# Optimization experiments

Measured on AMD Instinct MI355X. Metric: run time of the kernel, lower is better.

The kernel has to match this reference:

```python
import jax, jax.numpy as jnp
import numpy as np

NFEAT, NHID, NCLASS = 256, 128, 40
N_NODES, N_EDGES = 50000, 800000
BN_EPS = 1e-5


def setup_inputs() -> dict:
    key = jax.random.key(0)
    ks = jax.random.split(key, 8)
    x = jax.random.normal(ks[0], (N_NODES, NFEAT), dtype=jnp.float32)
    edge_index = jax.random.randint(ks[1], (2, N_EDGES), 0, N_NODES, dtype=jnp.int64)
    # GCNConv layer 0: nfeat -> nhid (Glorot-ish scale)
    W0 = jax.random.normal(ks[2], (NFEAT, NHID), dtype=jnp.float32) / np.sqrt(NFEAT)
    b0 = jnp.zeros((NHID,), dtype=jnp.float32)
    # BatchNorm1d(nhid)
    gamma0 = jnp.ones((NHID,), dtype=jnp.float32)
    beta0 = jnp.zeros((NHID,), dtype=jnp.float32)
    # GCNConv last: nhid -> nclass
    W1 = jax.random.normal(ks[3], (NHID, NCLASS), dtype=jnp.float32) / np.sqrt(NHID)
    b1 = jnp.zeros((NCLASS,), dtype=jnp.float32)
    return {"x": x, "edge_index": edge_index, "W0": W0, "b0": b0,
            "gamma0": gamma0, "beta0": beta0, "W1": W1, "b1": b1}


def _gcn_conv(x, src, dst, W, b, num_nodes):
    # normalize=False GCNConv: linear transform then raw sum aggregation src->dst
    h = x @ W                                   # [N, out]
    out = jax.ops.segment_sum(h[src], dst, num_segments=num_nodes)
    return out + b


def reference(x, edge_index, W0, b0, gamma0, beta0, W1, b1):
    N = x.shape[0]
    src, dst = edge_index[0], edge_index[1]
    # layer 0 conv
    h = _gcn_conv(x, src, dst, W0, b0, N)       # [N, nhid]
    # BatchNorm1d (training-mode batch stats, biased variance)
    mu = h.mean(axis=0)
    var = jnp.mean((h - mu) ** 2, axis=0)
    h = gamma0 * (h - mu) * jax.lax.rsqrt(var + BN_EPS) + beta0
    h = jax.nn.relu(h)
    # (dropout skipped: deterministic eval baseline)
    # last conv (early-return path in original forward)
    out = _gcn_conv(h, src, dst, W1, b1, N)     # [N, nclass]
    return out
```

## Files before the change

kernel.cpp:

```cpp
#include <hip/hip_runtime.h>
#include <hip/hip_fp8.h>

#define NFEAT 256
#define NHID 128
#define NCLASS 40
#define NNODES 50000
#define NEDGES 800000
#define BN_EPS 1e-5f
#define NBK 196
#define NBLK 100
#define EPB 8000
#define BKCAP 6144
#define NW1 6250
#define GEMM1_BLOCKS 1563

typedef __attribute__((ext_vector_type(4))) float f32x4;
typedef __attribute__((ext_vector_type(8))) short bf16x8;

__device__ inline ushort f2bf(float f) {
    uint u = __float_as_uint(f);
    u += 0x7FFF + ((u >> 16) & 1);
    return (ushort)(u >> 16);
}
__device__ inline float bflo(uint v) { return __uint_as_float(v << 16); }
__device__ inline float bfhi(uint v) { return __uint_as_float(v & 0xFFFF0000u); }

__device__ inline uint pk_fp8x4(float a0, float a1, float a2, float a3) {
#if __has_builtin(__builtin_amdgcn_cvt_pk_fp8_f32)
    int u = 0;
    u = __builtin_amdgcn_cvt_pk_fp8_f32(a0, a1, u, false);
    u = __builtin_amdgcn_cvt_pk_fp8_f32(a2, a3, u, true);
    return (uint)u;
#else
    __hip_fp8_e4m3 q0(a0), q1(a1), q2(a2), q3(a3);
    return (uint)q0.__x | ((uint)q1.__x << 8) | ((uint)q2.__x << 16) | ((uint)q3.__x << 24);
#endif
}
__device__ inline float fp8lo(uint v) {
#if __has_builtin(__builtin_amdgcn_cvt_f32_fp8)
    return __builtin_amdgcn_cvt_f32_fp8((int)v, 0);
#else
    __hip_fp8_e4m3 q; q.__x = (__hip_fp8_storage_t)(v & 0xFF); return (float)q;
#endif
}
__device__ inline float fp8hi(uint v) {
#if __has_builtin(__builtin_amdgcn_cvt_f32_fp8)
    return __builtin_amdgcn_cvt_f32_fp8((int)v, 1);
#else
    __hip_fp8_e4m3 q; q.__x = (__hip_fp8_storage_t)((v >> 8) & 0xFF); return (float)q;
#endif
}

__global__ void k_prep(const float* __restrict__ W0, ushort* __restrict__ W0F,
                       const int* __restrict__ ei, int* __restrict__ bcnt) {
    __shared__ int cnt[NBK];
    if (blockIdx.x < 16) {
        const int t = blockIdx.x * 256 + threadIdx.x;
        const int lane = t & 63;
        const int grp = t >> 6;
        const int kc = grp & 7, fi = grp >> 3;
        const int n = fi * 16 + (lane & 15);
        const int k0 = kc * 32 + (lane >> 4) * 8;
        ushort v[8];
        #pragma unroll
        for (int j = 0; j < 8; ++j) v[j] = f2bf(W0[(k0 + j) * NHID + n]);
        uint4 u;
        u.x = (uint)v[0] | ((uint)v[1] << 16);
        u.y = (uint)v[2] | ((uint)v[3] << 16);
        u.z = (uint)v[4] | ((uint)v[5] << 16);
        u.w = (uint)v[6] | ((uint)v[7] << 16);
        *(uint4*)&W0F[(grp * 64 + lane) * 8] = u;
    } else {
        const int blk = blockIdx.x - 16;
        const int t = threadIdx.x;
        if (t < NBK) cnt[t] = 0;
        __syncthreads();
        const int base = blk * EPB;
        for (int i = t; i < EPB; i += 256)
            atomicAdd(&cnt[ei[NEDGES + base + i] >> 8], 1);
        __syncthreads();
        if (t < NBK) bcnt[blk * NBK + t] = cnt[t];
    }
}

__global__ void k_bkscan(const int* __restrict__ bcnt, int* __restrict__ off,
                         int* __restrict__ bstart, int* __restrict__ rowptr,
                         float* __restrict__ stats) {
    __shared__ int sc[256];
    const int t = threadIdx.x;
    stats[t] = 0.f;
    int tot = 0;
    if (t < NBK)
        for (int b = 0; b < NBLK; ++b) tot += bcnt[b * NBK + t];
    sc[t] = tot;
    __syncthreads();
    for (int o = 1; o < 256; o <<= 1) {
        const int v = (t >= o) ? sc[t - o] : 0;
        __syncthreads();
        sc[t] += v;
        __syncthreads();
    }
    const int excl = sc[t] - tot;
    if (t < NBK) bstart[t] = excl;
    else if (t == NBK) bstart[NBK] = sc[NBK - 1];
    if (t == 0) rowptr[NNODES] = NEDGES;
    if (t < NBK) {
        int run = excl;
        for (int b = 0; b < NBLK; ++b) { off[b * NBK + t] = run; run += bcnt[b * NBK + t]; }
    }
}

__launch_bounds__(256)
__global__ void k_scatter_gemm1(const int* __restrict__ ei, const int* __restrict__ off,
                                uint* __restrict__ packed,
                                const float* __restrict__ x, const ushort* __restrict__ W0F,
                                uchar* __restrict__ h1) {
    __shared__ int cur[NBK];
    if (blockIdx.x < NBLK) {
        const int t = threadIdx.x, blk = blockIdx.x;
        if (t < NBK) cur[t] = off[blk * NBK + t];
        __syncthreads();
        const int base = blk * EPB;
        for (int i = t; i < EPB; i += 256) {
            const int src = ei[base + i];
            const int dst = ei[NEDGES + base + i];
            const int pos = atomicAdd(&cur[dst >> 8], 1);
            packed[pos] = (uint)src | ((uint)(dst & 255) << 16);
        }
    } else {
        const int gt = (blockIdx.x - NBLK) * 256 + threadIdx.x;
        const int w = gt >> 6;
        if (w >= NW1) return;
        const int lane = gt & 63;
        const int half = w & 1;
        const int node = (w >> 1) * 16 + (lane & 15);
        const int nclamp = node < NNODES ? node : NNODES - 1;
        const float* xg = &x[(long)nclamp * NFEAT + (lane >> 4) * 8];

        float4 xa[8], xb[8];
        #pragma unroll
        for (int kc = 0; kc < 8; ++kc) {
            xa[kc] = *(const float4*)(xg + kc * 32);
            xb[kc] = *(const float4*)(xg + kc * 32 + 4);
        }
        __builtin_amdgcn_sched_barrier(0);
        bf16x8 xf[8];
        #pragma unroll
        for (int kc = 0; kc < 8; ++kc) {
            xf[kc][0]=(short)f2bf(xa[kc].x); xf[kc][1]=(short)f2bf(xa[kc].y);
            xf[kc][2]=(short)f2bf(xa[kc].z); xf[kc][3]=(short)f2bf(xa[kc].w);
            xf[kc][4]=(short)f2bf(xb[kc].x); xf[kc][5]=(short)f2bf(xb[kc].y);
            xf[kc][6]=(short)f2bf(xb[kc].z); xf[kc][7]=(short)f2bf(xb[kc].w);
        }
        __builtin_amdgcn_sched_barrier(0);
        f32x4 acc[4];
        #pragma unroll
        for (int f = 0; f < 4; ++f) acc[f] = (f32x4){0.f, 0.f, 0.f, 0.f};
        const ushort* wbase = &W0F[(size_t)lane * 8];
        #pragma unroll
        for (int kc = 0; kc < 8; ++kc) {
            #pragma unroll
            for (int f = 0; f < 4; ++f) {
                const int grp = (half * 4 + f) * 8 + kc;
                const bf16x8 wf = *(const bf16x8*)&wbase[(size_t)grp * 64 * 8];
                acc[f] = __builtin_amdgcn_mfma_f32_16x16x32_bf16(wf, xf[kc], acc[f], 0, 0, 0);
            }
        }
        if (node < NNODES) {
            const int nq = (lane >> 4) * 4;
            uchar* hp = &h1[(long)node * NHID + half * 64 + nq];
            #pragma unroll
            for (int f = 0; f < 4; ++f)
                *(uint*)&hp[f * 16] = pk_fp8x4(acc[f][0], acc[f][1], acc[f][2], acc[f][3]);
        }
    }
}

__launch_bounds__(256)
__global__ void k_bksort(const uint* __restrict__ packed, const int* __restrict__ bstart,
                         int* __restrict__ esrc, int* __restrict__ rowptr) {
    __shared__ uint pr[BKCAP];
    __shared__ int cnt[256], sc[256], cur[256];
    const int t = threadIdx.x, b = blockIdx.x;
    const int nb = bstart[b], ne = bstart[b + 1];
    const int n = ne - nb;
    cnt[t] = 0;
    __syncthreads();
    for (int i = t; i < n; i += 256) {
        const uint p = packed[nb + i];
        pr[i] = p;
        atomicAdd(&cnt[p >> 16], 1);
    }
    __syncthreads();
    const int v = cnt[t];
    sc[t] = v;
    __syncthreads();
    for (int o = 1; o < 256; o <<= 1) {
        const int tmp = (t >= o) ? sc[t - o] : 0;
        __syncthreads();
        sc[t] += tmp;
        __syncthreads();
    }
    const int excl = sc[t] - v;
    cur[t] = excl;
    const int node = (b << 8) + t;
    if (node < NNODES) rowptr[node] = nb + excl;
    __syncthreads();
    for (int i = t; i < n; i += 256) {
        const uint p = pr[i];
        const int pos = atomicAdd(&cur[p >> 16], 1);
        esrc[nb + pos] = (int)(p & 0xFFFFu);
    }
}

__launch_bounds__(256)
__global__ void k_gather1(const int* __restrict__ rowptr, const int* __restrict__ esrc,
                          const uchar* __restrict__ h1, const float* __restrict__ b0,
                          float* __restrict__ agg1) {
    const int w = (blockIdx.x * blockDim.x + threadIdx.x) >> 6;
    const int lane = threadIdx.x & 63;
    if (w >= NNODES) return;
    const int beg = rowptr[w], end = rowptr[w + 1];
    const int f = lane * 2;
    float2 acc = *(const float2*)&b0[f];
    int i = beg;
    for (; i + 7 < end; i += 8) {
        uint v[8];
        #pragma unroll
        for (int j = 0; j < 8; ++j)
            v[j] = (uint)*(const ushort*)&h1[(long)esrc[i + j] * NHID + f];
        #pragma unroll
        for (int j = 0; j < 8; ++j) { acc.x += fp8lo(v[j]); acc.y += fp8hi(v[j]); }
    }
    for (; i < end; ++i) {
        const uint v = (uint)*(const ushort*)&h1[(long)esrc[i] * NHID + f];
        acc.x += fp8lo(v); acc.y += fp8hi(v);
    }
    *(float2*)&agg1[(long)w * NHID + f] = acc;
}

__global__ void k_bnstats(const float* __restrict__ agg1,
                          float* __restrict__ sums, float* __restrict__ sumsq) {
    __shared__ float sd[256 * 4], sd2[256 * 4];
    const int t = threadIdx.x;
    const int c4 = (t & 31) * 4;
    const int rr = t >> 5;
    float4 s = make_float4(0.f,0.f,0.f,0.f), s2 = s;
    for (int r = blockIdx.x * 8 + rr; r < NNODES; r += gridDim.x * 8) {
        const float4 v = *(const float4*)&agg1[(long)r * NHID + c4];
        s.x += v.x; s.y += v.y; s.z += v.z; s.w += v.w;
        s2.x += v.x*v.x; s2.y += v.y*v.y; s2.z += v.z*v.z; s2.w += v.w*v.w;
    }
    *(float4*)&sd[t * 4] = s; *(float4*)&sd2[t * 4] = s2;
    __syncthreads();
    if (t < 32) {
        #pragma unroll
        for (int j = 1; j < 8; ++j) {
            const float4 a = *(const float4*)&sd[(j * 32 + t) * 4];
            const float4 a2 = *(const float4*)&sd2[(j * 32 + t) * 4];
            s = *(float4*)&sd[t * 4];
            s2 = *(float4*)&sd2[t * 4];
            s.x += a.x; s.y += a.y; s.z += a.z; s.w += a.w;
            s2.x += a2.x; s2.y += a2.y; s2.z += a2.z; s2.w += a2.w;
            *(float4*)&sd[t * 4] = s; *(float4*)&sd2[t * 4] = s2;
        }
        atomicAdd(&sums[c4 + 0], s.x);  atomicAdd(&sums[c4 + 1], s.y);
        atomicAdd(&sums[c4 + 2], s.z);  atomicAdd(&sums[c4 + 3], s.w);
        atomicAdd(&sumsq[c4 + 0], s2.x); atomicAdd(&sumsq[c4 + 1], s2.y);
        atomicAdd(&sumsq[c4 + 2], s2.z); atomicAdd(&sumsq[c4 + 3], s2.w);
    }
}

__launch_bounds__(256)
__global__ void k_gemm2(const float* __restrict__ agg1, const float* __restrict__ W1,
                        const float* __restrict__ sums, const float* __restrict__ sumsq,
                        const float* __restrict__ gamma, const float* __restrict__ beta,
                        ushort* __restrict__ h2) {
    __shared__ float xs[64 * 132];
    __shared__ float wt[40 * 132];
    __shared__ float s_scale[128], s_shift[128];
    const int t = threadIdx.x;
    const int base = blockIdx.x * 64;

    if (t < NHID) {
        const float mu = sums[t] * (1.f / NNODES);
        float var = sumsq[t] * (1.f / NNODES) - mu * mu;
        var = fmaxf(var, 0.f);
        const float sc = gamma[t] * rsqrtf(var + BN_EPS);
        s_scale[t] = sc;
        s_shift[t] = beta[t] - mu * sc;
    }
    for (int idx = t; idx < NHID * NCLASS; idx += 256) {
        const int c = idx / NCLASS, j = idx % NCLASS;
        wt[j * 132 + c] = W1[idx];
    }
    __syncthreads();
    {
        const int cc = (t & 31) * 4;
        const float4 sc = *(const float4*)&s_scale[cc];
        const float4 sh = *(const float4*)&s_shift[cc];
        const int rb = t >> 5;
        #pragma unroll
        for (int p = 0; p < 8; ++p) {
            const int row = p * 8 + rb;
            const int g = base + row;
            float4 v = make_float4(0.f, 0.f, 0.f, 0.f);
            if (g < NNODES) {
                const float4 a = *(const float4*)&agg1[(long)g * NHID + cc];
                v.x = fmaxf(a.x * sc.x + sh.x, 0.f);
                v.y = fmaxf(a.y * sc.y + sh.y, 0.f);
                v.z = fmaxf(a.z * sc.z + sh.z, 0.f);
                v.w = fmaxf(a.w * sc.w + sh.w, 0.f);
            }
            *(float4*)&xs[row * 132 + cc] = v;
        }
    }
    __syncthreads();

    const int node = t >> 2;
    const int j0 = (t & 3) * 10;
    float acc[10] = {};
    for (int c4 = 0; c4 < 32; ++c4) {
        const int c = c4 * 4;
        const float4 a = *(const float4*)&xs[node * 132 + c];
        #pragma unroll
        for (int jj = 0; jj < 10; ++jj) {
            const float4 wv = *(const float4*)&wt[(j0 + jj) * 132 + c];
            acc[jj] += a.x * wv.x + a.y * wv.y + a.z * wv.z + a.w * wv.w;
        }
    }
    const int g = base + node;
    if (g < NNODES) {
        #pragma unroll
        for (int p = 0; p < 5; ++p) {
            uint u = (uint)f2bf(acc[2 * p]) | ((uint)f2bf(acc[2 * p + 1]) << 16);
            *(uint*)&h2[(long)g * NCLASS + j0 + 2 * p] = u;
        }
    }
}

__launch_bounds__(256)
__global__ void k_gather2(const int* __restrict__ rowptr, const int* __restrict__ esrc,
                          const ushort* __restrict__ h2, const float* __restrict__ b1,
                          float* __restrict__ out) {
    const int t = threadIdx.x;
    if (t >= 240) return;
    const int node = blockIdx.x * 12 + t / 20;
    if (node >= NNODES) return;
    const int f = (t % 20) * 2;
    const int beg = rowptr[node], end = rowptr[node + 1];
    float2 acc = make_float2(b1[f], b1[f + 1]);
    int i = beg;
    for (; i + 3 < end; i += 4) {
        const uint v0 = *(const uint*)&h2[(long)esrc[i]     * NCLASS + f];
        const uint v1 = *(const uint*)&h2[(long)esrc[i + 1] * NCLASS + f];
        const uint v2 = *(const uint*)&h2[(long)esrc[i + 2] * NCLASS + f];
        const uint v3 = *(const uint*)&h2[(long)esrc[i + 3] * NCLASS + f];
        acc.x += (bflo(v0) + bflo(v1)) + (bflo(v2) + bflo(v3));
        acc.y += (bfhi(v0) + bfhi(v1)) + (bfhi(v2) + bfhi(v3));
    }
    for (; i < end; ++i) {
        const uint v = *(const uint*)&h2[(long)esrc[i] * NCLASS + f];
        acc.x += bflo(v); acc.y += bfhi(v);
    }
    *(float2*)&out[(long)node * NCLASS + f] = acc;
}

extern "C" void kernel_launch(void* const* d_in, const int* in_sizes, int n_in,
                              void* d_out, int out_size, void* d_ws, size_t ws_size,
                              hipStream_t stream) {
    const float* x      = (const float*)d_in[0];
    const int*   ei     = (const int*)d_in[1];
    const float* W0     = (const float*)d_in[2];
    const float* b0     = (const float*)d_in[3];
    const float* gamma0 = (const float*)d_in[4];
    const float* beta0  = (const float*)d_in[5];
    const float* W1     = (const float*)d_in[6];
    const float* b1     = (const float*)d_in[7];
    float* out = (float*)d_out;

    char* ws = (char*)d_ws;
    float* sums  = (float*)ws;
    float* sumsq = sums + 128;
    int* wsI     = (int*)(ws + 4096);
    int* rowptr  = wsI;
    int* esrc    = wsI + 50048;
    int* bcnt    = wsI + 850048;
    int* off     = wsI + 869696;
    int* bstart  = wsI + 889344;
    ushort* W0F  = (ushort*)(ws + 3563520);
    uchar* h1    = (uchar*)(ws + 3629056);
    float* agg1  = (float*)(ws + 16429056);
    uint* packed = (uint*)agg1;
    ushort* h2   = (ushort*)h1;

    k_prep<<<16 + NBLK, 256, 0, stream>>>(W0, W0F, ei, bcnt);
    k_bkscan<<<1, 256, 0, stream>>>(bcnt, off, bstart, rowptr, sums);
    k_scatter_gemm1<<<NBLK + GEMM1_BLOCKS, 256, 0, stream>>>(ei, off, packed, x, W0F, h1);
    k_bksort<<<NBK, 256, 0, stream>>>(packed, bstart, esrc, rowptr);
    k_gather1<<<(NNODES * 64 + 255) / 256, 256, 0, stream>>>(rowptr, esrc, h1, b0, agg1);
    k_bnstats<<<256, 256, 0, stream>>>(agg1, sums, sumsq);
    k_gemm2<<<(NNODES + 63) / 64, 256, 0, stream>>>(agg1, W1, sums, sumsq, gamma0, beta0, h2);
    k_gather2<<<(NNODES + 11) / 12, 256, 0, stream>>>(rowptr, esrc, h2, b1, out);
}
```

Baseline: 169.4 us.

## Replace atomic bucket counting/scatter with per-thread byte-histogram stable counting sort

Replaces the shared-memory atomic histogram and atomic scatter in the edge bucketing and per-bucket sort with per-thread uint8 histograms in LDS, column prefix sums, and deterministic per-thread offsets. It doubles the number of counting blocks and halves edges per block, splits gemm1 out of the fused scatter kernel into its own launch, and launches one more kernel overall. The goal is to avoid LDS atomic contention and make CSR construction deterministic. In exchange it uses large LDS arrays (25–32KB per block), serial 128-row column scans, and relies on per-thread per-bucket counts fitting in a byte.

```diff
diff --git a/kernel.cpp b/kernel.cpp
--- a/kernel.cpp
+++ b/kernel.cpp
@@ -8,9 +8,8 @@
 #define NEDGES 800000
 #define BN_EPS 1e-5f
 #define NBK 196
-#define NBLK 100
-#define EPB 8000
-#define BKCAP 6144
+#define NBLK2 200
+#define EPB2 4000
 #define NW1 6250
 #define GEMM1_BLOCKS 1563
 
@@ -51,11 +50,11 @@
 #endif
 }
 
-__global__ void k_prep(const float* __restrict__ W0, ushort* __restrict__ W0F,
-                       const int* __restrict__ ei, int* __restrict__ bcnt) {
-    __shared__ int cnt[NBK];
-    if (blockIdx.x < 16) {
-        const int t = blockIdx.x * 256 + threadIdx.x;
+__launch_bounds__(128)
+__global__ void k_count(const int* __restrict__ ei, int* __restrict__ bcnt,
+                        const float* __restrict__ W0, ushort* __restrict__ W0F) {
+    if (blockIdx.x >= NBLK2) {
+        const int t = (blockIdx.x - NBLK2) * 128 + threadIdx.x;
         const int lane = t & 63;
         const int grp = t >> 6;
         const int kc = grp & 7, fi = grp >> 3;
@@ -70,16 +69,26 @@
         u.z = (uint)v[4] | ((uint)v[5] << 16);
         u.w = (uint)v[6] | ((uint)v[7] << 16);
         *(uint4*)&W0F[(grp * 64 + lane) * 8] = u;
-    } else {
-        const int blk = blockIdx.x - 16;
-        const int t = threadIdx.x;
-        if (t < NBK) cnt[t] = 0;
-        __syncthreads();
-        const int base = blk * EPB;
-        for (int i = t; i < EPB; i += 256)
-            atomicAdd(&cnt[ei[NEDGES + base + i] >> 8], 1);
-        __syncthreads();
-        if (t < NBK) bcnt[blk * NBK + t] = cnt[t];
+        return;
+    }
+    __shared__ uchar cnt8[128 * NBK];
+    const int t = threadIdx.x, blk = blockIdx.x;
+    for (int i = t * 4; i < 128 * NBK; i += 512) *(uint*)&cnt8[i] = 0u;
+    __syncthreads();
+    const int base = blk * EPB2;
+    #pragma unroll 4
+    for (int k = 0; k < 32; ++k) {
+        const int i = t + k * 128;
+        if (i < EPB2) {
+            const int b = ei[NEDGES + base + i] >> 8;
+            ++cnt8[t * NBK + b];
+        }
+    }
+    __syncthreads();
+    for (int c = t; c < NBK; c += 128) {
+        int s = 0;
+        for (int r = 0; r < 128; ++r) s += cnt8[r * NBK + c];
+        bcnt[blk * NBK + c] = s;
     }
 }
 
@@ -91,7 +100,7 @@
     stats[t] = 0.f;
     int tot = 0;
     if (t < NBK)
-        for (int b = 0; b < NBLK; ++b) tot += bcnt[b * NBK + t];
+        for (int b = 0; b < NBLK2; ++b) tot += bcnt[b * NBK + t];
     sc[t] = tot;
     __syncthreads();
     for (int o = 1; o < 256; o <<= 1) {
@@ -101,115 +110,158 @@
         __syncthreads();
     }
     const int excl = sc[t] - tot;
-    if (t < NBK) bstart[t] = excl;
-    else if (t == NBK) bstart[NBK] = sc[NBK - 1];
+    if (t <= NBK) bstart[t] = excl;
     if (t == 0) rowptr[NNODES] = NEDGES;
     if (t < NBK) {
         int run = excl;
-        for (int b = 0; b < NBLK; ++b) { off[b * NBK + t] = run; run += bcnt[b * NBK + t]; }
-    }
-}
-
-__launch_bounds__(256)
-__global__ void k_scatter_gemm1(const int* __restrict__ ei, const int* __restrict__ off,
-                                uint* __restrict__ packed,
-                                const float* __restrict__ x, const ushort* __restrict__ W0F,
-                                uchar* __restrict__ h1) {
-    __shared__ int cur[NBK];
-    if (blockIdx.x < NBLK) {
-        const int t = threadIdx.x, blk = blockIdx.x;
-        if (t < NBK) cur[t] = off[blk * NBK + t];
-        __syncthreads();
-        const int base = blk * EPB;
-        for (int i = t; i < EPB; i += 256) {
+        for (int b = 0; b < NBLK2; ++b) { off[b * NBK + t] = run; run += bcnt[b * NBK + t]; }
+    }
+}
+
+__launch_bounds__(128)
+__global__ void k_sortwrite(const int* __restrict__ ei, const int* __restrict__ off,
+                            uint* __restrict__ packed2) {
+    __shared__ uchar cnt8[128 * NBK];
+    __shared__ int offl[NBK];
+    const int t = threadIdx.x, blk = blockIdx.x;
+    for (int i = t * 4; i < 128 * NBK; i += 512) *(uint*)&cnt8[i] = 0u;
+    for (int c = t; c < NBK; c += 128) offl[c] = off[blk * NBK + c];
+    __syncthreads();
+    const int base = blk * EPB2;
+    #pragma unroll 4
+    for (int k = 0; k < 32; ++k) {
+        const int i = t + k * 128;
+        if (i < EPB2) {
+            const int b = ei[NEDGES + base + i] >> 8;
+            ++cnt8[t * NBK + b];
+        }
+    }
+    __syncthreads();
+    for (int c = t; c < NBK; c += 128) {
+        int run = 0;
+        for (int r = 0; r < 128; ++r) {
+            const int v = cnt8[r * NBK + c];
+            cnt8[r * NBK + c] = (uchar)run;
+            run += v;
+        }
+    }
+    __syncthreads();
+    #pragma unroll 4
+    for (int k = 0; k < 32; ++k) {
+        const int i = t + k * 128;
+        if (i < EPB2) {
             const int src = ei[base + i];
             const int dst = ei[NEDGES + base + i];
-            const int pos = atomicAdd(&cur[dst >> 8], 1);
-            packed[pos] = (uint)src | ((uint)(dst & 255) << 16);
-        }
-    } else {
-        const int gt = (blockIdx.x - NBLK) * 256 + threadIdx.x;
-        const int w = gt >> 6;
-        if (w >= NW1) return;
-        const int lane = gt & 63;
-        const int half = w & 1;
-        const int node = (w >> 1) * 16 + (lane & 15);
-        const int nclamp = node < NNODES ? node : NNODES - 1;
-        const float* xg = &x[(long)nclamp * NFEAT + (lane >> 4) * 8];
-
-        float4 xa[8], xb[8];
-        #pragma unroll
-        for (int kc = 0; kc < 8; ++kc) {
-            xa[kc] = *(const float4*)(xg + kc * 32);
-            xb[kc] = *(const float4*)(xg + kc * 32 + 4);
-        }
-        __builtin_amdgcn_sched_barrier(0);
-        bf16x8 xf[8];
-        #pragma unroll
-        for (int kc = 0; kc < 8; ++kc) {
-            xf[kc][0]=(short)f2bf(xa[kc].x); xf[kc][1]=(short)f2bf(xa[kc].y);
-            xf[kc][2]=(short)f2bf(xa[kc].z); xf[kc][3]=(short)f2bf(xa[kc].w);
-            xf[kc][4]=(short)f2bf(xb[kc].x); xf[kc][5]=(short)f2bf(xb[kc].y);
-            xf[kc][6]=(short)f2bf(xb[kc].z); xf[kc][7]=(short)f2bf(xb[kc].w);
-        }
-        __builtin_amdgcn_sched_barrier(0);
-        f32x4 acc[4];
-        #pragma unroll
-        for (int f = 0; f < 4; ++f) acc[f] = (f32x4){0.f, 0.f, 0.f, 0.f};
-        const ushort* wbase = &W0F[(size_t)lane * 8];
-        #pragma unroll
-        for (int kc = 0; kc < 8; ++kc) {
-            #pragma unroll
-            for (int f = 0; f < 4; ++f) {
-                const int grp = (half * 4 + f) * 8 + kc;
-                const bf16x8 wf = *(const bf16x8*)&wbase[(size_t)grp * 64 * 8];
-                acc[f] = __builtin_amdgcn_mfma_f32_16x16x32_bf16(wf, xf[kc], acc[f], 0, 0, 0);
-            }
-        }
-        if (node < NNODES) {
-            const int nq = (lane >> 4) * 4;
-            uchar* hp = &h1[(long)node * NHID + half * 64 + nq];
-            #pragma unroll
-            for (int f = 0; f < 4; ++f)
-                *(uint*)&hp[f * 16] = pk_fp8x4(acc[f][0], acc[f][1], acc[f][2], acc[f][3]);
-        }
-    }
-}
-
-__launch_bounds__(256)
-__global__ void k_bksort(const uint* __restrict__ packed, const int* __restrict__ bstart,
+            const int b = dst >> 8;
+            const int lp = cnt8[t * NBK + b];
+            cnt8[t * NBK + b] = (uchar)(lp + 1);
+            packed2[offl[b] + lp] = (uint)src | ((uint)(dst & 255) << 16);
+        }
+    }
+}
+
+__launch_bounds__(128)
+__global__ void k_bksort(const uint* __restrict__ packed2, const int* __restrict__ bstart,
                          int* __restrict__ esrc, int* __restrict__ rowptr) {
-    __shared__ uint pr[BKCAP];
-    __shared__ int cnt[256], sc[256], cur[256];
+    __shared__ uchar cnt8[128 * 256];
+    __shared__ int nodebase[257];
     const int t = threadIdx.x, b = blockIdx.x;
     const int nb = bstart[b], ne = bstart[b + 1];
     const int n = ne - nb;
-    cnt[t] = 0;
-    __syncthreads();
-    for (int i = t; i < n; i += 256) {
-        const uint p = packed[nb + i];
-        pr[i] = p;
-        atomicAdd(&cnt[p >> 16], 1);
-    }
-    __syncthreads();
-    const int v = cnt[t];
-    sc[t] = v;
-    __syncthreads();
-    for (int o = 1; o < 256; o <<= 1) {
-        const int tmp = (t >= o) ? sc[t - o] : 0;
-        __syncthreads();
-        sc[t] += tmp;
-        __syncthreads();
-    }
-    const int excl = sc[t] - v;
-    cur[t] = excl;
-    const int node = (b << 8) + t;
-    if (node < NNODES) rowptr[node] = nb + excl;
-    __syncthreads();
-    for (int i = t; i < n; i += 256) {
-        const uint p = pr[i];
-        const int pos = atomicAdd(&cur[p >> 16], 1);
-        esrc[nb + pos] = (int)(p & 0xFFFFu);
+    {
+        uint4* z = (uint4*)cnt8;
+        const uint4 zz = make_uint4(0u, 0u, 0u, 0u);
+        for (int i = t; i < 2048; i += 128) z[i] = zz;
+    }
+    __syncthreads();
+    const int kmax = (n + 127) >> 7;
+    for (int k = 0; k < kmax; ++k) {
+        const int i = t + k * 128;
+        if (i < n) {
+            const uint p = packed2[nb + i];
+            ++cnt8[t * 256 + (p >> 16)];
+        }
+    }
+    __syncthreads();
+    for (int c = t; c < 256; c += 128) {
+        int run = 0;
+        for (int r = 0; r < 128; ++r) {
+            const int v = cnt8[r * 256 + c];
+            cnt8[r * 256 + c] = (uchar)run;
+            run += v;
+        }
+        nodebase[c] = run;
+    }
+    __syncthreads();
+    if (t == 0) {
+        int run = 0;
+        for (int c = 0; c < 256; ++c) { const int v = nodebase[c]; nodebase[c] = run; run += v; }
+        nodebase[256] = run;
+    }
+    __syncthreads();
+    for (int c = t; c < 256; c += 128) {
+        const int node = (b << 8) + c;
+        if (node < NNODES) rowptr[node] = nb + nodebase[c];
+    }
+    for (int k = 0; k < kmax; ++k) {
+        const int i = t + k * 128;
+        if (i < n) {
+            const uint p = packed2[nb + i];
+            const int nd = (int)(p >> 16);
+            const int lp = cnt8[t * 256 + nd];
+            cnt8[t * 256 + nd] = (uchar)(lp + 1);
+            esrc[nb + nodebase[nd] + lp] = (int)(p & 0xFFFFu);
+        }
+    }
+}
+
+__launch_bounds__(256)
+__global__ void k_gemm1(const float* __restrict__ x, const ushort* __restrict__ W0F,
+                        uchar* __restrict__ h1) {
+    const int gt = blockIdx.x * 256 + threadIdx.x;
+    const int w = gt >> 6;
+    if (w >= NW1) return;
+    const int lane = gt & 63;
+    const int half = w & 1;
+    const int node = (w >> 1) * 16 + (lane & 15);
+    const int nclamp = node < NNODES ? node : NNODES - 1;
+    const float* xg = &x[(long)nclamp * NFEAT + (lane >> 4) * 8];
+
+    float4 xa[8], xb[8];
+    #pragma unroll
+    for (int kc = 0; kc < 8; ++kc) {
+        xa[kc] = *(const float4*)(xg + kc * 32);
+        xb[kc] = *(const float4*)(xg + kc * 32 + 4);
+    }
+    __builtin_amdgcn_sched_barrier(0);
+    bf16x8 xf[8];
+    #pragma unroll
+    for (int kc = 0; kc < 8; ++kc) {
+        xf[kc][0]=(short)f2bf(xa[kc].x); xf[kc][1]=(short)f2bf(xa[kc].y);
+        xf[kc][2]=(short)f2bf(xa[kc].z); xf[kc][3]=(short)f2bf(xa[kc].w);
+        xf[kc][4]=(short)f2bf(xb[kc].x); xf[kc][5]=(short)f2bf(xb[kc].y);
+        xf[kc][6]=(short)f2bf(xb[kc].z); xf[kc][7]=(short)f2bf(xb[kc].w);
+    }
+    __builtin_amdgcn_sched_barrier(0);
+    f32x4 acc[4];
+    #pragma unroll
+    for (int f = 0; f < 4; ++f) acc[f] = (f32x4){0.f, 0.f, 0.f, 0.f};
+    const ushort* wbase = &W0F[(size_t)lane * 8];
+    #pragma unroll
+    for (int kc = 0; kc < 8; ++kc) {
+        #pragma unroll
+        for (int f = 0; f < 4; ++f) {
+            const int grp = (half * 4 + f) * 8 + kc;
+            const bf16x8 wf = *(const bf16x8*)&wbase[(size_t)grp * 64 * 8];
+            acc[f] = __builtin_amdgcn_mfma_f32_16x16x32_bf16(wf, xf[kc], acc[f], 0, 0, 0);
+        }
+    }
+    if (node < NNODES) {
+        const int nq = (lane >> 4) * 4;
+        uchar* hp = &h1[(long)node * NHID + half * 64 + nq];
+        #pragma unroll
+        for (int f = 0; f < 4; ++f)
+            *(uint*)&hp[f * 16] = pk_fp8x4(acc[f][0], acc[f][1], acc[f][2], acc[f][3]);
     }
 }
 
@@ -386,18 +438,19 @@
     int* rowptr  = wsI;
     int* esrc    = wsI + 50048;
     int* bcnt    = wsI + 850048;
-    int* off     = wsI + 869696;
-    int* bstart  = wsI + 889344;
-    ushort* W0F  = (ushort*)(ws + 3563520);
-    uchar* h1    = (uchar*)(ws + 3629056);
+    int* off     = wsI + 889344;
+    int* bstart  = wsI + 928640;
+    ushort* W0F  = (ushort*)(ws + 3720192);
+    uchar* h1    = (uchar*)(ws + 3785728);
     float* agg1  = (float*)(ws + 16429056);
-    uint* packed = (uint*)agg1;
+    uint* packed2 = (uint*)agg1;
     ushort* h2   = (ushort*)h1;
 
-    k_prep<<<16 + NBLK, 256, 0, stream>>>(W0, W0F, ei, bcnt);
+    k_count<<<NBLK2 + 32, 128, 0, stream>>>(ei, bcnt, W0, W0F);
     k_bkscan<<<1, 256, 0, stream>>>(bcnt, off, bstart, rowptr, sums);
-    k_scatter_gemm1<<<NBLK + GEMM1_BLOCKS, 256, 0, stream>>>(ei, off, packed, x, W0F, h1);
-    k_bksort<<<NBK, 256, 0, stream>>>(packed, bstart, esrc, rowptr);
+    k_sortwrite<<<NBLK2, 128, 0, stream>>>(ei, off, packed2);
+    k_bksort<<<NBK, 128, 0, stream>>>(packed2, bstart, esrc, rowptr);
+    k_gemm1<<<GEMM1_BLOCKS, 256, 0, stream>>>(x, W0F, h1);
     k_gather1<<<(NNODES * 64 + 255) / 256, 256, 0, stream>>>(rowptr, esrc, h1, b0, agg1);
     k_bnstats<<<256, 256, 0, stream>>>(agg1, sums, sumsq);
     k_gemm2<<<(NNODES + 63) / 64, 256, 0, stream>>>(agg1, W1, sums, sumsq, gamma0, beta0, h2);
```

Result: slower. 211.9 us (+25.0%).
